# Optimization experiments

Hardware: AMD Instinct MI355X
Metric: run time of the kernel (lower is better)

Reference implementation:

```python
import jax, jax.numpy as jnp
import numpy as np

D_MODEL = 1024
N_HEADS = 16
DH = D_MODEL // N_HEADS
ROPE_THETA = 10000.0


def rotate_half(u):
    h = u.shape[-1] // 2
    return jnp.concatenate([-u[..., h:], u[..., :h]], axis=-1)


def apply_rope(q, k, cos, sin):
    return q * cos + rotate_half(q) * sin, k * cos + rotate_half(k) * sin


def setup_inputs() -> dict:
    key = jax.random.key(0)
    ks = jax.random.split(key, 6)
    B, S = 2, 2048
    x = jax.random.normal(ks[0], (B, S, D_MODEL), dtype=jnp.float32)
    y = jax.random.normal(ks[1], (B, S, D_MODEL), dtype=jnp.float32)
    wq = 0.01 * jax.random.normal(ks[2], (D_MODEL, D_MODEL), dtype=jnp.float32)
    wk = 0.01 * jax.random.normal(ks[3], (D_MODEL, D_MODEL), dtype=jnp.float32)
    wv = 0.01 * jax.random.normal(ks[4], (D_MODEL, D_MODEL), dtype=jnp.float32)
    wo = 0.01 * jax.random.normal(ks[5], (D_MODEL, D_MODEL), dtype=jnp.float32)
    return {"x": x, "y": y, "wq": wq, "wk": wk, "wv": wv, "wo": wo}


def reference(x, y, wq, wk, wv, wo):
    B, S, D = x.shape
    past_length = 0  # default; kv_cache=None

    Q = x @ wq.T                      # (B,S,D)
    K = y                             # NOTE: K is y un-projected (as in source)
    V = y @ wv.T
    # K1 = x @ wk.T is computed in the source but immediately overwritten
    # by the buggy second apply_rope call -> wk is unused in the output.
    V1 = x @ wo.T

    def heads(t):
        return t.reshape(B, S, N_HEADS, DH).transpose(0, 2, 1, 3)  # (B,H,S,dh)

    q_h, k_h, v_h, v1_h = heads(Q), heads(K), heads(V), heads(V1)

    # RoPE tables (past_length:past_length+S rows of the cache)
    freqs = 1.0 / ROPE_THETA ** (jnp.arange(0, DH, 2, dtype=jnp.float32) / DH)
    emb = jnp.arange(past_length, past_length + S, dtype=jnp.float32)[:, None] * freqs[None, :]
    cos = jnp.concatenate([jnp.cos(emb), jnp.cos(emb)], axis=-1)[None, None]  # (1,1,S,dh)
    sin = jnp.concatenate([jnp.sin(emb), jnp.sin(emb)], axis=-1)[None, None]

    q_h, k_h = apply_rope(q_h, k_h, cos, sin)
    # faithful to source: k1 = rope applied AGAIN to the already-roped k
    _, k1_h = apply_rope(q_h, k_h, cos, sin)

    k_full = jnp.concatenate([k_h, k1_h], axis=2)   # (B,H,2S,dh)
    v_full = jnp.concatenate([v_h, v1_h], axis=2)
    S_full = k_full.shape[2]

    # mask: tril(diagonal=past_length) over (S,S_full), last S cols = eye(S)
    rows = jnp.arange(S)[:, None]
    cols = jnp.arange(S_full)[None, :]
    mask = cols <= rows + past_length
    mask = mask.at[:, -S:].set(jnp.eye(S, dtype=bool))  # (S,S_full)

    scores = jnp.einsum("bhqd,bhkd->bhqk", q_h, k_full) / jnp.sqrt(jnp.asarray(DH, x.dtype))
    scores = jnp.where(mask[None, None], scores, jnp.asarray(-1e30, x.dtype))
    attn = jax.nn.softmax(scores, axis=-1)
    out = jnp.einsum("bhqk,bhkd->bhqd", attn, v_full)
    out = out.transpose(0, 2, 1, 3).reshape(B, S, D)

    k_ret = k_full[:, :, :-S, :]
    return out, k_ret
```

## Files before the change

### kernel.cpp

```cpp
#include <hip/hip_runtime.h>

#define DM 1024
#define NHEADS 16
#define DHEAD 64
#define BB 2
#define SS 2048
#define BH (BB*NHEADS)

typedef __attribute__((ext_vector_type(8))) short short8;
typedef __attribute__((ext_vector_type(4))) float float4v;
typedef unsigned short ushort_t;

#define LN1E4_D32 0.28782313662425572f
#define SM_SCALE  0.18033688011112042f

static __device__ __forceinline__ unsigned short f2bf(float f) {
    union { float f; unsigned u; } v; v.f = f;
    unsigned r = v.u + 0x7fffu + ((v.u >> 16) & 1u);
    return (unsigned short)(r >> 16);
}
static __device__ __forceinline__ float bf2f(unsigned short u) {
    union { float f; unsigned u; } v; v.u = ((unsigned)u) << 16;
    return v.f;
}
static __device__ __forceinline__ unsigned cvtpk_bf16(float lo, float hi) {
    unsigned r;
    asm("v_cvt_pk_bf16_f32 %0, %1, %2" : "=v"(r) : "v"(lo), "v"(hi));
    return r;
}
static __device__ __forceinline__ float ex2(float x) {
    float r;
    asm("v_exp_f32 %0, %1" : "=v"(r) : "v"(x));
    return r;
}

static __device__ __forceinline__ void gload16(const ushort_t* g, ushort_t* l) {
    __builtin_amdgcn_global_load_lds(
        (const __attribute__((address_space(1))) void*)g,
        (__attribute__((address_space(3))) void*)l, 16, 0, 0);
}

__global__ __launch_bounds__(256) void prep_kernel(
        const float* __restrict__ x, const float* __restrict__ y,
        const float* __restrict__ wq, const float* __restrict__ wv,
        const float* __restrict__ wo,
        ushort_t* __restrict__ xb, ushort_t* __restrict__ wqb,
        ushort_t* __restrict__ wvb, ushort_t* __restrict__ wob,
        float* __restrict__ kout, ushort_t* __restrict__ khb,
        ushort_t* __restrict__ yb) {
    if (blockIdx.x < 3584) {
        int C = blockIdx.x * 256 + threadIdx.x;
        int c  = C & 511;
        int tl = C >> 9;
        int rb = tl >> 5, kb = tl & 31;
        const float* src; ushort_t* dst; int r0;
        if (rb < 32)      { src = x;  r0 = rb * 128;        dst = xb  + (size_t)tl * 4096; }
        else if (rb < 40) { src = wq; r0 = (rb - 32) * 128; dst = wqb + (size_t)(((rb - 32) * 32) + kb) * 4096; }
        else if (rb < 48) { src = wv; r0 = (rb - 40) * 128; dst = wvb + (size_t)(((rb - 40) * 32) + kb) * 4096; }
        else              { src = wo; r0 = (rb - 48) * 128; dst = wob + (size_t)(((rb - 48) * 32) + kb) * 4096; }
        int row = c >> 2, g = c & 3;
        int kk3 = g ^ ((row >> 1) & 3);
        const float* s = src + (size_t)(r0 + row) * DM + kb * 32 + kk3 * 8;
        float4 a0 = *reinterpret_cast<const float4*>(s);
        float4 a1 = *reinterpret_cast<const float4*>(s + 4);
        short8 v;
        v[0] = (short)f2bf(a0.x); v[1] = (short)f2bf(a0.y);
        v[2] = (short)f2bf(a0.z); v[3] = (short)f2bf(a0.w);
        v[4] = (short)f2bf(a1.x); v[5] = (short)f2bf(a1.y);
        v[6] = (short)f2bf(a1.z); v[7] = (short)f2bf(a1.w);
        *reinterpret_cast<short8*>(dst + c * 8) = v;
        return;
    }
    int t = (blockIdx.x - 3584) * 256 + threadIdx.x;
    int i8 = t & 3;
    int s  = (t >> 2) & (SS - 1);
    int bh = t >> 13;
    int h = bh & (NHEADS - 1), b = bh >> 4;

    const float* yp = y + ((size_t)(b * SS + s)) * DM + h * DHEAD + i8 * 8;
    float4 a0 = *reinterpret_cast<const float4*>(yp);
    float4 a1 = *reinterpret_cast<const float4*>(yp + 4);
    float4 b0 = *reinterpret_cast<const float4*>(yp + 32);
    float4 b1 = *reinterpret_cast<const float4*>(yp + 36);
    float u0[8] = {a0.x, a0.y, a0.z, a0.w, a1.x, a1.y, a1.z, a1.w};
    float u1[8] = {b0.x, b0.y, b0.z, b0.w, b1.x, b1.y, b1.z, b1.w};
    float lo[8], hi[8];
#pragma unroll
    for (int j = 0; j < 8; j++) {
        int i = i8 * 8 + j;
        float freq = __expf(-(float)i * LN1E4_D32);
        float th = (float)s * freq;
        float cv, sv;
        __sincosf(th, &sv, &cv);
        lo[j] = u0[j] * cv - u1[j] * sv;
        hi[j] = u1[j] * cv + u0[j] * sv;
    }
    float* op = kout + ((size_t)bh * SS + s) * DHEAD + i8 * 8;
    *reinterpret_cast<float4*>(op)      = (float4){lo[0], lo[1], lo[2], lo[3]};
    *reinterpret_cast<float4*>(op + 4)  = (float4){lo[4], lo[5], lo[6], lo[7]};
    *reinterpret_cast<float4*>(op + 32) = (float4){hi[0], hi[1], hi[2], hi[3]};
    *reinterpret_cast<float4*>(op + 36) = (float4){hi[4], hi[5], hi[6], hi[7]};

    ushort_t* kb = khb + ((size_t)bh * 32 + (s >> 6)) * 4096 + (s & 63) * 64;
    short8 vlo, vhi;
#pragma unroll
    for (int j = 0; j < 8; j++) { vlo[j] = (short)f2bf(lo[j]); vhi[j] = (short)f2bf(hi[j]); }
    *reinterpret_cast<short8*>(kb + ((i8 ^ (s & 7)) << 3))       = vlo;
    *reinterpret_cast<short8*>(kb + (((i8 + 4) ^ (s & 7)) << 3)) = vhi;

    int rowm = b * SS + s;
    int rowin = rowm & 127, rbm = rowm >> 7;
    int g = i8 ^ ((rowin >> 1) & 3);
    ushort_t* yt = yb + ((size_t)(rbm * 32 + h * 2)) * 4096 + rowin * 32 + (g << 3);
    short8 ulo, uhi;
#pragma unroll
    for (int j = 0; j < 8; j++) { ulo[j] = (short)f2bf(u0[j]); uhi[j] = (short)f2bf(u1[j]); }
    *reinterpret_cast<short8*>(yt)        = ulo;
    *reinterpret_cast<short8*>(yt + 4096) = uhi;
}

__global__ __launch_bounds__(256, 2) void gemm3_kernel(
        const ushort_t* __restrict__ xb, const ushort_t* __restrict__ yb,
        const ushort_t* __restrict__ wqb, const ushort_t* __restrict__ wvb,
        const ushort_t* __restrict__ wob,
        ushort_t* __restrict__ qh, ushort_t* __restrict__ vt, ushort_t* __restrict__ v1h) {
    __shared__ __align__(16) char smem[34816];
    ushort_t* As = (ushort_t*)smem;
    ushort_t* Bs = (ushort_t*)(smem + 16384);
    ushort_t (*Ct)[136] = (ushort_t(*)[136])smem;

    int bid = blockIdx.x;
    int xcd = bid & 7;
    int s_  = bid >> 3;
    int zo  = s_ >> 5;
    int z   = (zo == 0) ? 0 : (zo == 1 ? 2 : 1);
    int t_  = s_ & 31;
    int n0  = (t_ >> 2) * 128;
    int m0  = (xcd * 4 + (t_ & 3)) * 128;

    const ushort_t* A = (z == 1) ? yb : xb;
    const ushort_t* W = (z == 0) ? wqb : (z == 1 ? wvb : wob);
    ushort_t* O = (z == 0) ? qh : (z == 1 ? vt : v1h);

    const ushort_t* Atl = A + (size_t)(m0 >> 7) * 32 * 4096;
    const ushort_t* Wtl = W + (size_t)(n0 >> 7) * 32 * 4096;

    int tid = threadIdx.x;
    int wave = tid >> 6, lane = tid & 63, quad = lane >> 4, l15 = lane & 15;
    int wr = (wave >> 1) * 64, wc = (wave & 1) * 64;

    int gi0 = tid * 8, gi1 = (256 + tid) * 8;
    int li0 = (tid & 192) * 8, li1 = (256 + (tid & 192)) * 8;

    int aoff[4], boff[4];
#pragma unroll
    for (int mi = 0; mi < 4; mi++) {
        int row = wr + mi * 16 + l15;
        aoff[mi] = row * 32 + ((quad ^ ((row >> 1) & 3)) << 3);
    }
#pragma unroll
    for (int ni = 0; ni < 4; ni++) {
        int row = wc + ni * 16 + l15;
        boff[ni] = row * 32 + ((quad ^ ((row >> 1) & 3)) << 3);
    }

    float4v acc[4][4];
#pragma unroll
    for (int a = 0; a < 4; a++)
#pragma unroll
        for (int b = 0; b < 4; b++)
            acc[a][b] = (float4v){0.f, 0.f, 0.f, 0.f};

    gload16(Atl + gi0, As + li0); gload16(Atl + gi1, As + li1);
    gload16(Wtl + gi0, Bs + li0); gload16(Wtl + gi1, Bs + li1);
    int cur = 0;

    for (int kb = 0; kb < 32; kb++) {
        __syncthreads();
        if (kb + 1 < 32) {
            const ushort_t* at = Atl + (size_t)(kb + 1) * 4096;
            const ushort_t* wt = Wtl + (size_t)(kb + 1) * 4096;
            int nb = (cur ^ 1) * 4096;
            gload16(at + gi0, As + nb + li0); gload16(at + gi1, As + nb + li1);
            gload16(wt + gi0, Bs + nb + li0); gload16(wt + gi1, Bs + nb + li1);
        }
        const ushort_t* Ac = As + cur * 4096;
        const ushort_t* Bc = Bs + cur * 4096;
        short8 af[4], bfr[4];
#pragma unroll
        for (int mi = 0; mi < 4; mi++)
            af[mi] = *reinterpret_cast<const short8*>(&Ac[aoff[mi]]);
#pragma unroll
        for (int ni = 0; ni < 4; ni++)
            bfr[ni] = *reinterpret_cast<const short8*>(&Bc[boff[ni]]);
#pragma unroll
        for (int mi = 0; mi < 4; mi++)
#pragma unroll
            for (int ni = 0; ni < 4; ni++)
                acc[mi][ni] = __builtin_amdgcn_mfma_f32_16x16x32_bf16(af[mi], bfr[ni], acc[mi][ni], 0, 0, 0);
        cur ^= 1;
    }

    if (z == 0) {
#pragma unroll
        for (int mi = 0; mi < 4; mi++)
#pragma unroll
            for (int r = 0; r < 4; r++) {
                int m = m0 + wr + mi * 16 + quad * 4 + r;
                float pos = (float)(m & (SS - 1));
#pragma unroll
                for (int ni = 0; ni < 2; ni++) {
                    int d = ni * 16 + l15;
                    float f = __expf(-(float)d * LN1E4_D32);
                    float th = pos * f;
                    float cv, sv;
                    __sincosf(th, &sv, &cv);
                    cv *= SM_SCALE; sv *= SM_SCALE;
                    float u0 = acc[mi][ni][r], u1 = acc[mi][ni + 2][r];
                    acc[mi][ni][r]     = u0 * cv - u1 * sv;
                    acc[mi][ni + 2][r] = u1 * cv + u0 * sv;
                }
            }
    }

    __syncthreads();
#pragma unroll
    for (int mi = 0; mi < 4; mi++)
#pragma unroll
        for (int ni = 0; ni < 4; ni++) {
            int col = wc + ni * 16 + l15;
#pragma unroll
            for (int r = 0; r < 4; r++)
                Ct[wr + mi * 16 + quad * 4 + r][col] = f2bf(acc[mi][ni][r]);
        }
    __syncthreads();
    int h0 = n0 >> 6;
    if (z == 1) {
        int b = m0 >> 11;
        int s0 = m0 & (SS - 1);
#pragma unroll
        for (int it = 0; it < 8; it++) {
            int c = it * 256 + tid;
            int dh  = c & 63;
            int k16 = (c >> 6) & 15;
            int hh  = c >> 10;
            short8 v;
#pragma unroll
            for (int e = 0; e < 8; e++)
                v[e] = (short)Ct[k16 * 8 + e][hh * 64 + dh];
            int kt = (s0 >> 6) + (k16 >> 3);
            size_t off = ((size_t)((b * NHEADS + h0 + hh) * 32 + kt)) * 4096
                       + dh * 64 + (((k16 & 7) ^ (dh & 7)) << 3);
            *reinterpret_cast<short8*>(&O[off]) = v;
        }
    } else {
#pragma unroll
        for (int it = 0; it < 8; it++) {
            int c = it * 256 + tid;
            int o = c >> 3, j = c & 7;
            int hh = o >> 7, mr = o & 127;
            int m = m0 + mr, b = m >> 11, si = m & (SS - 1);
            uint4 v = *reinterpret_cast<const uint4*>(&Ct[mr][hh * 64 + j * 8]);
            *reinterpret_cast<uint4*>(
                &O[((size_t)((b * NHEADS + h0 + hh) * SS + si)) * DHEAD + j * 8]) = v;
        }
    }
}

template<bool MASKED>
static __device__ __forceinline__ void attn_tile(
        const ushort_t* __restrict__ Kc, const ushort_t* __restrict__ Vc, int kbase,
        int quad, int l15, int q0w, const short8* qf, const short8& onesf,
        ushort_t* __restrict__ Psw, float4v* Oa, float4v& sum4) {
    float4v sa[4];
#pragma unroll
    for (int t2 = 0; t2 < 4; t2++) sa[t2] = (float4v){0.f, 0.f, 0.f, 0.f};
    __builtin_amdgcn_s_setprio(1);
#pragma unroll
    for (int t2 = 0; t2 < 4; t2++) {
        int key = t2 * 16 + l15;
        int ro = key * 64, sw = key & 7;
#pragma unroll
        for (int half = 0; half < 2; half++) {
            short8 kf = *reinterpret_cast<const short8*>(&Kc[ro + (((half * 4 + quad) ^ sw) << 3)]);
            sa[t2] = __builtin_amdgcn_mfma_f32_16x16x32_bf16(kf, qf[half], sa[t2], 0, 0, 0);
        }
    }
    __builtin_amdgcn_s_setprio(0);
    int query = q0w + l15;
    int swl = l15 & 7;
#pragma unroll
    for (int t2 = 0; t2 < 4; t2++) {
        float p[4];
#pragma unroll
        for (int r = 0; r < 4; r++) {
            float e = ex2(sa[t2][r]);
            if (MASKED) {
                int key = kbase + t2 * 16 + quad * 4 + r;
                p[r] = (key <= query) ? e : 0.f;
            } else {
                p[r] = e;
            }
        }
        unsigned w0 = cvtpk_bf16(p[0], p[1]);
        unsigned w1 = cvtpk_bf16(p[2], p[3]);
        int chunk = (((t2 * 2 + (quad >> 1)) ^ swl) << 3) + (quad & 1) * 4;
        *reinterpret_cast<unsigned*>(&Psw[l15 * 64 + chunk])     = w0;
        *reinterpret_cast<unsigned*>(&Psw[l15 * 64 + chunk + 2]) = w1;
    }
    short8 pf0 = *reinterpret_cast<const short8*>(&Psw[l15 * 64 + ((quad ^ swl) << 3)]);
    short8 pf1 = *reinterpret_cast<const short8*>(&Psw[l15 * 64 + (((4 + quad) ^ swl) << 3)]);
    __builtin_amdgcn_s_setprio(1);
#pragma unroll
    for (int t = 0; t < 4; t++) {
        int dh = t * 16 + l15;
        int ro = dh * 64, sw = dh & 7;
        short8 vf0 = *reinterpret_cast<const short8*>(&Vc[ro + ((quad ^ sw) << 3)]);
        short8 vf1 = *reinterpret_cast<const short8*>(&Vc[ro + (((4 + quad) ^ sw) << 3)]);
        Oa[t] = __builtin_amdgcn_mfma_f32_16x16x32_bf16(pf0, vf0, Oa[t], 0, 0, 0);
        Oa[t] = __builtin_amdgcn_mfma_f32_16x16x32_bf16(pf1, vf1, Oa[t], 0, 0, 0);
    }
    sum4 = __builtin_amdgcn_mfma_f32_16x16x32_bf16(pf0, onesf, sum4, 0, 0, 0);
    sum4 = __builtin_amdgcn_mfma_f32_16x16x32_bf16(pf1, onesf, sum4, 0, 0, 0);
    __builtin_amdgcn_s_setprio(0);
}

__global__ __launch_bounds__(512, 4) void attn_kernel(
        const ushort_t* __restrict__ qh, const float* __restrict__ kf32,
        const ushort_t* __restrict__ khb, const ushort_t* __restrict__ vtb,
        const ushort_t* __restrict__ v1h, float* __restrict__ out) {
    __shared__ __align__(16) ushort_t Ks[4][4096];
    __shared__ __align__(16) ushort_t Vt[4][4096];
    __shared__ __align__(16) ushort_t Ps[8][1024];

    int bid = blockIdx.x;
    int bh = (bid & 7) * 4 + ((bid >> 3) & 3);
    int p  = bid >> 5;

    int tid = threadIdx.x, wave = tid >> 6, lane = tid & 63, quad = lane >> 4, l15 = lane & 15;
    int jq  = (wave < 4) ? p : (31 - p);
    int q0w = jq * 64 + (wave & 3) * 16;
    const ushort_t* qp  = qh  + (size_t)bh * SS * DHEAD;
    const float*    kp  = kf32 + (size_t)bh * SS * DHEAD;
    const ushort_t* v1p = v1h + (size_t)bh * SS * DHEAD;
    const ushort_t* ktb = khb + (size_t)bh * 32 * 4096;
    const ushort_t* vtt = vtb + (size_t)bh * 32 * 4096;

    short8 qf[2];
    qf[0] = *reinterpret_cast<const short8*>(&qp[(q0w + l15) * DHEAD + quad * 8]);
    qf[1] = *reinterpret_cast<const short8*>(&qp[(q0w + l15) * DHEAD + 32 + quad * 8]);
    short8 onesf;
#pragma unroll
    for (int j = 0; j < 8; j++) onesf[j] = (short)0x3F80;

    float4v Oa[4];
#pragma unroll
    for (int t = 0; t < 4; t++) Oa[t] = (float4v){0.f, 0.f, 0.f, 0.f};
    float4v sum4 = (float4v){0.f, 0.f, 0.f, 0.f};

    int gi = tid * 8;
    int li = (tid & 448) * 8;

    int ntiles = 32 - p;
    gload16(ktb + gi, &Ks[0][li]);               gload16(vtt + gi, &Vt[0][li]);
    gload16(ktb + 4096 + gi, &Ks[1][li]);        gload16(vtt + 4096 + gi, &Vt[1][li]);

    int kt = 0;
    for (; kt + 1 < ntiles; kt += 2) {
        __syncthreads();
        if (kt + 2 < ntiles) {
            const ushort_t* gk = ktb + (size_t)(kt + 2) * 4096;
            const ushort_t* gv = vtt + (size_t)(kt + 2) * 4096;
            int nb = (kt + 2) & 3;
            gload16(gk + gi, &Ks[nb][li]);
            gload16(gv + gi, &Vt[nb][li]);
        }
        if (kt + 3 < ntiles) {
            const ushort_t* gk = ktb + (size_t)(kt + 3) * 4096;
            const ushort_t* gv = vtt + (size_t)(kt + 3) * 4096;
            int nb = (kt + 3) & 3;
            gload16(gk + gi, &Ks[nb][li]);
            gload16(gv + gi, &Vt[nb][li]);
        }
        {
            int kbase = kt * 64, sl = kt & 3;
            if (kbase <= q0w + 15) {
                if (kbase + 63 <= q0w)
                    attn_tile<false>(Ks[sl], Vt[sl], kbase, quad, l15, q0w, qf, onesf,
                                     &Ps[wave][0], Oa, sum4);
                else
                    attn_tile<true>(Ks[sl], Vt[sl], kbase, quad, l15, q0w, qf, onesf,
                                    &Ps[wave][0], Oa, sum4);
            }
        }
        {
            int kbase = (kt + 1) * 64, sl = (kt + 1) & 3;
            if (kbase <= q0w + 15) {
                if (kbase + 63 <= q0w)
                    attn_tile<false>(Ks[sl], Vt[sl], kbase, quad, l15, q0w, qf, onesf,
                                     &Ps[wave][0], Oa, sum4);
                else
                    attn_tile<true>(Ks[sl], Vt[sl], kbase, quad, l15, q0w, qf, onesf,
                                    &Ps[wave][0], Oa, sum4);
            }
        }
    }
    if (kt < ntiles) {
        __syncthreads();
        int kbase = kt * 64, sl = kt & 3;
        if (kbase <= q0w + 15) {
            if (kbase + 63 <= q0w)
                attn_tile<false>(Ks[sl], Vt[sl], kbase, quad, l15, q0w, qf, onesf,
                                 &Ps[wave][0], Oa, sum4);
            else
                attn_tile<true>(Ks[sl], Vt[sl], kbase, quad, l15, q0w, qf, onesf,
                                &Ps[wave][0], Oa, sum4);
        }
    }

    float* sdiag = reinterpret_cast<float*>(&Ps[wave][32]);

    {
        int sk = q0w + l15;
        const float* krow = kp + (size_t)sk * DHEAD;
        short8 k1lo, k1hi;
#pragma unroll
        for (int j = 0; j < 8; j++) {
            int d = quad * 8 + j;
            float f = __expf(-(float)d * LN1E4_D32);
            float th = (float)sk * f;
            float cv, sv;
            __sincosf(th, &sv, &cv);
            float a = krow[d], b2 = krow[d + 32];
            k1lo[j] = (short)f2bf(a * cv - b2 * sv);
            k1hi[j] = (short)f2bf(b2 * cv + a * sv);
        }
        float4v sd4 = (float4v){0.f, 0.f, 0.f, 0.f};
        sd4 = __builtin_amdgcn_mfma_f32_16x16x32_bf16(qf[0], k1lo, sd4, 0, 0, 0);
        sd4 = __builtin_amdgcn_mfma_f32_16x16x32_bf16(qf[1], k1hi, sd4, 0, 0, 0);
#pragma unroll
        for (int r = 0; r < 4; r++)
            if (l15 == quad * 4 + r) sdiag[l15] = sd4[r];

        int b = bh >> 4, h = bh & (NHEADS - 1);
#pragma unroll
        for (int r = 0; r < 4; r++) {
            float pd = ex2(sdiag[quad * 4 + r]);
            int query = q0w + quad * 4 + r;
            float linv = 1.f / (sum4[r] + pd);
#pragma unroll
            for (int t = 0; t < 4; t++) {
                float v1v = bf2f(v1p[query * DHEAD + t * 16 + l15]);
                float o = (Oa[t][r] + pd * v1v) * linv;
                out[(b * SS + query) * DM + h * DHEAD + t * 16 + l15] = o;
            }
        }
    }
}

extern "C" void kernel_launch(void* const* d_in, const int* in_sizes, int n_in,
                              void* d_out, int out_size, void* d_ws, size_t ws_size,
                              hipStream_t stream) {
    const float* x  = (const float*)d_in[0];
    const float* y  = (const float*)d_in[1];
    const float* wq = (const float*)d_in[2];
    const float* wv = (const float*)d_in[4];
    const float* wo = (const float*)d_in[5];
    float* outp  = (float*)d_out;
    float* k_out = outp + (size_t)BB * SS * DM;

    char* ws = (char*)d_ws;
    ushort_t* vtb = (ushort_t*)(ws);
    ushort_t* v1b = (ushort_t*)(ws + (8ull  << 20));
    ushort_t* qhb = (ushort_t*)(ws + (16ull << 20));
    ushort_t* khb = (ushort_t*)(ws + (24ull << 20));
    ushort_t* xb  = (ushort_t*)(ws + (32ull << 20));
    ushort_t* yb  = (ushort_t*)(ws + (40ull << 20));
    ushort_t* wqb = (ushort_t*)(ws + (48ull << 20));
    ushort_t* wvb = (ushort_t*)(ws + (50ull << 20));
    ushort_t* wob = (ushort_t*)(ws + (52ull << 20));

    prep_kernel<<<4608, 256, 0, stream>>>(x, y, wq, wv, wo, xb, wqb, wvb, wob,
                                          k_out, khb, yb);
    gemm3_kernel<<<768, 256, 0, stream>>>(xb, yb, wqb, wvb, wob, qhb, vtb, v1b);
    attn_kernel<<<512, 512, 0, stream>>>(qhb, k_out, khb, vtb, v1b, outp);
}
```

Measured before the change: 167.5 us.

## Merge Q and V1 projections into one GEMM block sharing the x tile

The x-side projections (Q with wq and V1 with wo) are now computed by the same block. Each loaded x tile feeds two MFMA chains into two accumulator sets, so x is read from global memory once instead of twice. The grid drops from 768 to 512 blocks, with half of them doing double work. In exchange, register use doubles to 128 accumulator floats and LDS grows to 48KB. This risks lower occupancy under launch_bounds(256,2) and leaves the merged and V blocks with unequal amounts of work.

```diff
diff --git a/kernel.cpp b/kernel.cpp
--- a/kernel.cpp
+++ b/kernel.cpp
@@ -124,26 +124,26 @@
         const ushort_t* __restrict__ wqb, const ushort_t* __restrict__ wvb,
         const ushort_t* __restrict__ wob,
         ushort_t* __restrict__ qh, ushort_t* __restrict__ vt, ushort_t* __restrict__ v1h) {
-    __shared__ __align__(16) char smem[34816];
+    __shared__ __align__(16) char smem[49152];
     ushort_t* As = (ushort_t*)smem;
     ushort_t* Bs = (ushort_t*)(smem + 16384);
+    ushort_t* Cs = (ushort_t*)(smem + 32768);
     ushort_t (*Ct)[136] = (ushort_t(*)[136])smem;
 
     int bid = blockIdx.x;
     int xcd = bid & 7;
     int s_  = bid >> 3;
-    int zo  = s_ >> 5;
-    int z   = (zo == 0) ? 0 : (zo == 1 ? 2 : 1);
+    int merged = (s_ < 32);
     int t_  = s_ & 31;
     int n0  = (t_ >> 2) * 128;
     int m0  = (xcd * 4 + (t_ & 3)) * 128;
 
-    const ushort_t* A = (z == 1) ? yb : xb;
-    const ushort_t* W = (z == 0) ? wqb : (z == 1 ? wvb : wob);
-    ushort_t* O = (z == 0) ? qh : (z == 1 ? vt : v1h);
-
-    const ushort_t* Atl = A + (size_t)(m0 >> 7) * 32 * 4096;
-    const ushort_t* Wtl = W + (size_t)(n0 >> 7) * 32 * 4096;
+    const ushort_t* A  = merged ? xb : yb;
+    const ushort_t* W1 = merged ? wqb : wvb;
+
+    const ushort_t* Atl = A   + (size_t)(m0 >> 7) * 32 * 4096;
+    const ushort_t* W1t = W1  + (size_t)(n0 >> 7) * 32 * 4096;
+    const ushort_t* W2t = wob + (size_t)(n0 >> 7) * 32 * 4096;
 
     int tid = threadIdx.x;
     int wave = tid >> 6, lane = tid & 63, quad = lane >> 4, l15 = lane & 15;
@@ -164,44 +164,64 @@
         boff[ni] = row * 32 + ((quad ^ ((row >> 1) & 3)) << 3);
     }
 
-    float4v acc[4][4];
+    float4v acc1[4][4], acc2[4][4];
 #pragma unroll
     for (int a = 0; a < 4; a++)
 #pragma unroll
-        for (int b = 0; b < 4; b++)
-            acc[a][b] = (float4v){0.f, 0.f, 0.f, 0.f};
+        for (int b = 0; b < 4; b++) {
+            acc1[a][b] = (float4v){0.f, 0.f, 0.f, 0.f};
+            acc2[a][b] = (float4v){0.f, 0.f, 0.f, 0.f};
+        }
 
     gload16(Atl + gi0, As + li0); gload16(Atl + gi1, As + li1);
-    gload16(Wtl + gi0, Bs + li0); gload16(Wtl + gi1, Bs + li1);
+    gload16(W1t + gi0, Bs + li0); gload16(W1t + gi1, Bs + li1);
+    if (merged) { gload16(W2t + gi0, Cs + li0); gload16(W2t + gi1, Cs + li1); }
     int cur = 0;
 
     for (int kb = 0; kb < 32; kb++) {
         __syncthreads();
         if (kb + 1 < 32) {
             const ushort_t* at = Atl + (size_t)(kb + 1) * 4096;
-            const ushort_t* wt = Wtl + (size_t)(kb + 1) * 4096;
+            const ushort_t* w1 = W1t + (size_t)(kb + 1) * 4096;
             int nb = (cur ^ 1) * 4096;
             gload16(at + gi0, As + nb + li0); gload16(at + gi1, As + nb + li1);
-            gload16(wt + gi0, Bs + nb + li0); gload16(wt + gi1, Bs + nb + li1);
+            gload16(w1 + gi0, Bs + nb + li0); gload16(w1 + gi1, Bs + nb + li1);
+            if (merged) {
+                const ushort_t* w2 = W2t + (size_t)(kb + 1) * 4096;
+                gload16(w2 + gi0, Cs + nb + li0); gload16(w2 + gi1, Cs + nb + li1);
+            }
         }
         const ushort_t* Ac = As + cur * 4096;
         const ushort_t* Bc = Bs + cur * 4096;
-        short8 af[4], bfr[4];
+        const ushort_t* Cc = Cs + cur * 4096;
+        short8 af[4], b1[4];
 #pragma unroll
         for (int mi = 0; mi < 4; mi++)
             af[mi] = *reinterpret_cast<const short8*>(&Ac[aoff[mi]]);
 #pragma unroll
         for (int ni = 0; ni < 4; ni++)
-            bfr[ni] = *reinterpret_cast<const short8*>(&Bc[boff[ni]]);
+            b1[ni] = *reinterpret_cast<const short8*>(&Bc[boff[ni]]);
 #pragma unroll
         for (int mi = 0; mi < 4; mi++)
 #pragma unroll
             for (int ni = 0; ni < 4; ni++)
-                acc[mi][ni] = __builtin_amdgcn_mfma_f32_16x16x32_bf16(af[mi], bfr[ni], acc[mi][ni], 0, 0, 0);
+                acc1[mi][ni] = __builtin_amdgcn_mfma_f32_16x16x32_bf16(af[mi], b1[ni], acc1[mi][ni], 0, 0, 0);
+        if (merged) {
+            short8 b2[4];
+#pragma unroll
+            for (int ni = 0; ni < 4; ni++)
+                b2[ni] = *reinterpret_cast<const short8*>(&Cc[boff[ni]]);
+#pragma unroll
+            for (int mi = 0; mi < 4; mi++)
+#pragma unroll
+                for (int ni = 0; ni < 4; ni++)
+                    acc2[mi][ni] = __builtin_amdgcn_mfma_f32_16x16x32_bf16(af[mi], b2[ni], acc2[mi][ni], 0, 0, 0);
+        }
         cur ^= 1;
     }
 
-    if (z == 0) {
+    int h0 = n0 >> 6;
+    if (merged) {
 #pragma unroll
         for (int mi = 0; mi < 4; mi++)
 #pragma unroll
@@ -216,44 +236,22 @@
                     float cv, sv;
                     __sincosf(th, &sv, &cv);
                     cv *= SM_SCALE; sv *= SM_SCALE;
-                    float u0 = acc[mi][ni][r], u1 = acc[mi][ni + 2][r];
-                    acc[mi][ni][r]     = u0 * cv - u1 * sv;
-                    acc[mi][ni + 2][r] = u1 * cv + u0 * sv;
+                    float u0 = acc1[mi][ni][r], u1 = acc1[mi][ni + 2][r];
+                    acc1[mi][ni][r]     = u0 * cv - u1 * sv;
+                    acc1[mi][ni + 2][r] = u1 * cv + u0 * sv;
                 }
             }
-    }
-
-    __syncthreads();
-#pragma unroll
-    for (int mi = 0; mi < 4; mi++)
-#pragma unroll
-        for (int ni = 0; ni < 4; ni++) {
-            int col = wc + ni * 16 + l15;
-#pragma unroll
-            for (int r = 0; r < 4; r++)
-                Ct[wr + mi * 16 + quad * 4 + r][col] = f2bf(acc[mi][ni][r]);
-        }
-    __syncthreads();
-    int h0 = n0 >> 6;
-    if (z == 1) {
-        int b = m0 >> 11;
-        int s0 = m0 & (SS - 1);
-#pragma unroll
-        for (int it = 0; it < 8; it++) {
-            int c = it * 256 + tid;
-            int dh  = c & 63;
-            int k16 = (c >> 6) & 15;
-            int hh  = c >> 10;
-            short8 v;
-#pragma unroll
-            for (int e = 0; e < 8; e++)
-                v[e] = (short)Ct[k16 * 8 + e][hh * 64 + dh];
-            int kt = (s0 >> 6) + (k16 >> 3);
-            size_t off = ((size_t)((b * NHEADS + h0 + hh) * 32 + kt)) * 4096
-                       + dh * 64 + (((k16 & 7) ^ (dh & 7)) << 3);
-            *reinterpret_cast<short8*>(&O[off]) = v;
-        }
-    } else {
+        __syncthreads();
+#pragma unroll
+        for (int mi = 0; mi < 4; mi++)
+#pragma unroll
+            for (int ni = 0; ni < 4; ni++) {
+                int col = wc + ni * 16 + l15;
+#pragma unroll
+                for (int r = 0; r < 4; r++)
+                    Ct[wr + mi * 16 + quad * 4 + r][col] = f2bf(acc1[mi][ni][r]);
+            }
+        __syncthreads();
 #pragma unroll
         for (int it = 0; it < 8; it++) {
             int c = it * 256 + tid;
@@ -262,7 +260,57 @@
             int m = m0 + mr, b = m >> 11, si = m & (SS - 1);
             uint4 v = *reinterpret_cast<const uint4*>(&Ct[mr][hh * 64 + j * 8]);
             *reinterpret_cast<uint4*>(
-                &O[((size_t)((b * NHEADS + h0 + hh) * SS + si)) * DHEAD + j * 8]) = v;
+                &qh[((size_t)((b * NHEADS + h0 + hh) * SS + si)) * DHEAD + j * 8]) = v;
+        }
+        __syncthreads();
+#pragma unroll
+        for (int mi = 0; mi < 4; mi++)
+#pragma unroll
+            for (int ni = 0; ni < 4; ni++) {
+                int col = wc + ni * 16 + l15;
+#pragma unroll
+                for (int r = 0; r < 4; r++)
+                    Ct[wr + mi * 16 + quad * 4 + r][col] = f2bf(acc2[mi][ni][r]);
+            }
+        __syncthreads();
+#pragma unroll
+        for (int it = 0; it < 8; it++) {
+            int c = it * 256 + tid;
+            int o = c >> 3, j = c & 7;
+            int hh = o >> 7, mr = o & 127;
+            int m = m0 + mr, b = m >> 11, si = m & (SS - 1);
+            uint4 v = *reinterpret_cast<const uint4*>(&Ct[mr][hh * 64 + j * 8]);
+            *reinterpret_cast<uint4*>(
+                &v1h[((size_t)((b * NHEADS + h0 + hh) * SS + si)) * DHEAD + j * 8]) = v;
+        }
+    } else {
+        __syncthreads();
+#pragma unroll
+        for (int mi = 0; mi < 4; mi++)
+#pragma unroll
+            for (int ni = 0; ni < 4; ni++) {
+                int col = wc + ni * 16 + l15;
+#pragma unroll
+                for (int r = 0; r < 4; r++)
+                    Ct[wr + mi * 16 + quad * 4 + r][col] = f2bf(acc1[mi][ni][r]);
+            }
+        __syncthreads();
+        int b = m0 >> 11;
+        int s0 = m0 & (SS - 1);
+#pragma unroll
+        for (int it = 0; it < 8; it++) {
+            int c = it * 256 + tid;
+            int dh  = c & 63;
+            int k16 = (c >> 6) & 15;
+            int hh  = c >> 10;
+            short8 v;
+#pragma unroll
+            for (int e = 0; e < 8; e++)
+                v[e] = (short)Ct[k16 * 8 + e][hh * 64 + dh];
+            int kt = (s0 >> 6) + (k16 >> 3);
+            size_t off = ((size_t)((b * NHEADS + h0 + hh) * 32 + kt)) * 4096
+                       + dh * 64 + (((k16 & 7) ^ (dh & 7)) << 3);
+            *reinterpret_cast<short8*>(&vt[off]) = v;
         }
     }
 }
@@ -482,6 +530,6 @@
 
     prep_kernel<<<4608, 256, 0, stream>>>(x, y, wq, wv, wo, xb, wqb, wvb, wob,
                                           k_out, khb, yb);
-    gemm3_kernel<<<768, 256, 0, stream>>>(xb, yb, wqb, wvb, wob, qhb, vtb, v1b);
+    gemm3_kernel<<<512, 256, 0, stream>>>(xb, yb, wqb, wvb, wob, qhb, vtb, v1b);
     attn_kernel<<<512, 512, 0, stream>>>(qhb, k_out, khb, vtb, v1b, outp);
 }
```

Result: no change. 167.5 us, median of 2 (+0.0%).
